# Performance work log

Hardware: AMD Instinct MI355X
Metric: run time of the kernel (lower is better)

Reference implementation:

```python
import jax, jax.numpy as jnp
import numpy as np

# Config values (from c.mean_shift / c.cuda in the original module)
EMBED_DIM = 32      # embedding_dim
BW = 2.0            # kernel_bandwidth
ETA = 0.5           # step_size
N_ITERS = 3         # nb_iterations
RES = 96            # pic_res (image is RES x RES, N = RES*RES pixels)


def setup_inputs() -> dict:
    key = jax.random.key(0)
    # Scale 0.1 keeps exp(BW * x^T x) well inside fp32 range, mimicking the
    # bounded embeddings produced by the upstream margin-loss-trained net.
    x_in = 0.1 * jax.random.normal(key, (1, EMBED_DIM, RES, RES), dtype=jnp.float32)
    return {"x_in": x_in}


def reference(x_in):
    # x_in: (1, D, RES, RES). One mean-shift step per iteration:
    #   K = exp(bw * X^T X)                      (N x N affinity)
    #   deg_j = sum_i K[i, j]                    (column degree; K is symmetric)
    #   X_new = eta * X @ (K / deg) + (1-eta) * X
    # (The original's torch.inverse(diag(deg)) is exactly 1/deg column scaling.)
    # All iterates are concatenated along dim 0, as in the torch code.
    res = x_in.shape[3]
    n = res * res
    xs = [x_in.reshape(EMBED_DIM, n)]
    for _ in range(N_ITERS):
        X = xs[-1]                                    # (D, N)
        K = jnp.exp(BW * jnp.einsum('di,dj->ij', X, X))  # (N, N)
        deg = K.sum(axis=0)                           # (N,) column sums
        xs.append(ETA * (X @ (K / deg)) + (1.0 - ETA) * X)
    # (N_ITERS+1, D, RES, RES)
    return jnp.stack(xs, axis=0).reshape(-1, EMBED_DIM, res, res)
```

## Files before the change

kernel.cpp:

```cpp
#include <hip/hip_runtime.h>
#include <hip/hip_bf16.h>


#define DIM 32
#define RESO 96
#define NPT (RESO * RESO)
#define NITER 3
#define ETA 0.5f
#define SCALE 2.88539008f

#define QB 144
#define NQB (NPT / QB)
#define NG 9
#define KSEG 4
#define CHUNK 256
#define NCHUNK (NPT / CHUNK)

typedef __bf16 bf16_t;
typedef __bf16 v8bf __attribute__((ext_vector_type(8)));
typedef float  v4f  __attribute__((ext_vector_type(4)));

__device__ __forceinline__ int keyinv(int m) {
    return ((m & 8) << 1) | ((m & 4) << 1) | ((m & 16) >> 2) | (m & 3);
}

__global__ __launch_bounds__(256, 4)
void pack_kernel(const float* __restrict__ X,
                 bf16_t* __restrict__ rows,
                 bf16_t* __restrict__ rows_s,
                 bf16_t* __restrict__ cols,
                 float* __restrict__ out_copy) {
    __shared__ float tt[32][33];
    const int tid = threadIdx.x;
    const int n0  = blockIdx.x * 32;
    const int inv = keyinv(tid & 31);

#pragma unroll
    for (int j = 0; j < 4; ++j) {
        int d = (tid >> 5) + j * 8;
        int n = tid & 31;
        float v = X[(size_t)d * NPT + n0 + n];
        tt[d][n] = v;
        cols[(size_t)d * NPT + n0 + inv] = (bf16_t)v;
        out_copy[(size_t)d * NPT + n0 + n] = v;
    }
    __syncthreads();

#pragma unroll
    for (int j = 0; j < 4; ++j) {
        int n = (tid >> 5) + j * 8;
        int d = tid & 31;
        float v = tt[d][n];
        rows[(size_t)(n0 + n) * DIM + d]   = (bf16_t)v;
        rows_s[(size_t)(n0 + n) * DIM + d] = (bf16_t)(v * SCALE);
    }
}

__global__ __launch_bounds__(512, 2)
void msattn_kernel(const bf16_t* __restrict__ rows,
                   const bf16_t* __restrict__ rows_s,
                   const bf16_t* __restrict__ cols,
                   float* __restrict__ part_num,
                   float* __restrict__ part_den) {
    __shared__ float osum[8][48][33];
    __shared__ float dsum[8][QB];

    const int tid  = threadIdx.x;
    const int w    = tid >> 6;
    const int lane = tid & 63;
    const int quad = lane >> 4;
    const int l16  = lane & 15;
    const int qb   = blockIdx.x;
    const int ks   = blockIdx.y;
    const int c0   = ks * (NCHUNK / KSEG);
    const int c1   = c0 + (NCHUNK / KSEG);
    const int q0   = qb * QB;

    v8bf qf[NG];
#pragma unroll
    for (int g = 0; g < NG; ++g)
        qf[g] = *(const v8bf*)&rows_s[(size_t)(q0 + g * 16 + l16) * DIM + quad * 8];

    v8bf ones;
#pragma unroll
    for (int j = 0; j < 8; ++j) ones[j] = (bf16_t)1.0f;

    const bf16_t* pA = rows + ((size_t)(c0 * CHUNK + w * 32 + l16)) * DIM + quad * 8;
    const bf16_t* pB = cols + (size_t)l16 * NPT + c0 * CHUNK + w * 32 + quad * 8;

    v4f acc[NG][2];
    v4f den[NG];
#pragma unroll
    for (int g = 0; g < NG; ++g) {
        acc[g][0] = (v4f){0.f, 0.f, 0.f, 0.f};
        acc[g][1] = (v4f){0.f, 0.f, 0.f, 0.f};
        den[g]    = (v4f){0.f, 0.f, 0.f, 0.f};
    }

    v8bf ka0 = *(const v8bf*)pA;
    v8bf ka1 = *(const v8bf*)(pA + 16 * DIM);
    v8bf bV0 = *(const v8bf*)pB;
    v8bf bV1 = *(const v8bf*)(pB + (size_t)16 * NPT);
    pA += CHUNK * DIM;
    pB += CHUNK;

    for (int c = c0; c < c1; ++c) {
        const bool more = (c + 1 < c1);
        v8bf nka0, nka1, nb0, nb1;
        if (more) {
            nka0 = *(const v8bf*)pA;
            nka1 = *(const v8bf*)(pA + 16 * DIM);
            nb0  = *(const v8bf*)pB;
            nb1  = *(const v8bf*)(pB + (size_t)16 * NPT);
            pA += CHUNK * DIM;
            pB += CHUNK;
        }

#pragma unroll
        for (int g = 0; g < NG; ++g) {
            v4f s0 = __builtin_amdgcn_mfma_f32_16x16x32_bf16(ka0, qf[g],
                         (v4f){0.f, 0.f, 0.f, 0.f}, 0, 0, 0);
            v4f s1 = __builtin_amdgcn_mfma_f32_16x16x32_bf16(ka1, qf[g],
                         (v4f){0.f, 0.f, 0.f, 0.f}, 0, 0, 0);
            v8bf pa;
#pragma unroll
            for (int r = 0; r < 4; ++r) {
                pa[r]     = (bf16_t)__builtin_amdgcn_exp2f(s0[r]);
                pa[4 + r] = (bf16_t)__builtin_amdgcn_exp2f(s1[r]);
            }
            acc[g][0] = __builtin_amdgcn_mfma_f32_16x16x32_bf16(pa, bV0, acc[g][0], 0, 0, 0);
            acc[g][1] = __builtin_amdgcn_mfma_f32_16x16x32_bf16(pa, bV1, acc[g][1], 0, 0, 0);
            den[g]    = __builtin_amdgcn_mfma_f32_16x16x32_bf16(pa, ones, den[g], 0, 0, 0);
        }

        if (more) { ka0 = nka0; ka1 = nka1; bV0 = nb0; bV1 = nb1; }
    }

    if (l16 == 0) {
#pragma unroll
        for (int g = 0; g < NG; ++g)
#pragma unroll
            for (int r = 0; r < 4; ++r)
                dsum[w][g * 16 + quad * 4 + r] = den[g][r];
    }

#pragma unroll
    for (int round = 0; round < 3; ++round) {
        if (round) __syncthreads();
#pragma unroll
        for (int gg = 0; gg < 3; ++gg) {
            int g = round * 3 + gg;
#pragma unroll
            for (int h = 0; h < 2; ++h)
#pragma unroll
                for (int r = 0; r < 4; ++r)
                    osum[w][gg * 16 + quad * 4 + r][h * 16 + l16] = acc[g][h][r];
        }
        __syncthreads();
#pragma unroll
        for (int e = 0; e < 3; ++e) {
            int idx = tid + e * 512;
            int qr = idx >> 5, d = idx & 31;
            float s = osum[0][qr][d] + osum[1][qr][d] + osum[2][qr][d]
                    + osum[3][qr][d] + osum[4][qr][d] + osum[5][qr][d]
                    + osum[6][qr][d] + osum[7][qr][d];
            part_num[((size_t)ks * NPT + q0 + round * 48 + qr) * DIM + d] = s;
        }
    }
    if (tid < QB) {
        float s = dsum[0][tid] + dsum[1][tid] + dsum[2][tid] + dsum[3][tid]
                + dsum[4][tid] + dsum[5][tid] + dsum[6][tid] + dsum[7][tid];
        part_den[ks * NPT + q0 + tid] = s;
    }
}

__global__ __launch_bounds__(512, 2)
void reduce_kernel(const float* __restrict__ part_num,
                   const float* __restrict__ part_den,
                   const float* __restrict__ Xcur,
                   float* __restrict__ Xnext,
                   bf16_t* __restrict__ rows_out,
                   bf16_t* __restrict__ rows_s_out,
                   bf16_t* __restrict__ cols_out) {
    __shared__ float tp[2][32][33];
    __shared__ float dpart[KSEG][32];
    __shared__ float txn[32][33];

    const int tid = threadIdx.x;
    const int q0  = blockIdx.x * 32;
    const int inv = keyinv(tid & 31);

    {
        int slot = tid & 255;
        int sh   = tid >> 8;
        int qq = slot >> 3, dq = slot & 7;
        const float* pb = &part_num[(size_t)(q0 + qq) * DIM + dq * 4];
        size_t seg = (size_t)NPT * DIM;
        v4f s = *(const v4f*)&pb[(2 * sh) * seg]
              + *(const v4f*)&pb[(2 * sh + 1) * seg];
#pragma unroll
        for (int k = 0; k < 4; ++k) tp[sh][qq][dq * 4 + k] = s[k];
    }
    if (tid < KSEG * 32) {
        int ss = tid >> 5, q = tid & 31;
        dpart[ss][q] = part_den[ss * NPT + q0 + q];
    }
    __syncthreads();

#pragma unroll
    for (int e = 0; e < 2; ++e) {
        int idx = tid + e * 512;
        int d = idx >> 5, qq = idx & 31;
        float num = tp[0][qq][d] + tp[1][qq][d];
        float dn = dpart[0][qq] + dpart[1][qq] + dpart[2][qq] + dpart[3][qq];
        float xo = Xcur[(size_t)d * NPT + q0 + qq];
        float xn = ETA * num / dn + (1.0f - ETA) * xo;
        Xnext[(size_t)d * NPT + q0 + qq] = xn;
        cols_out[(size_t)d * NPT + q0 + inv] = (bf16_t)xn;
        txn[qq][d] = xn;
    }
    __syncthreads();

#pragma unroll
    for (int e = 0; e < 2; ++e) {
        int idx = tid + e * 512;
        int qq = idx >> 5, d = idx & 31;
        float v = txn[qq][d];
        rows_out[(size_t)(q0 + qq) * DIM + d]   = (bf16_t)v;
        rows_s_out[(size_t)(q0 + qq) * DIM + d] = (bf16_t)(v * SCALE);
    }
}

extern "C" void kernel_launch(void* const* d_in, const int* in_sizes, int n_in,
                              void* d_out, int out_size, void* d_ws, size_t ws_size,
                              hipStream_t stream) {
    const float* x_in = (const float*)d_in[0];
    float* out = (float*)d_out;

    const size_t DN = (size_t)DIM * NPT;
    bf16_t* rows0  = (bf16_t*)d_ws;
    bf16_t* rowss0 = rows0 + DN;
    bf16_t* cols0  = rowss0 + DN;
    bf16_t* rows1  = cols0 + DN;
    bf16_t* rowss1 = rows1 + DN;
    bf16_t* cols1  = rowss1 + DN;
    float* part_num = (float*)(cols1 + DN);
    float* part_den = part_num + (size_t)KSEG * NPT * DIM;

    pack_kernel<<<NPT / 32, 256, 0, stream>>>(x_in, rows0, rowss0, cols0, out);

    for (int it = 0; it < NITER; ++it) {
        const float* Xcur = (it == 0) ? x_in : out + (size_t)it * DN;
        bf16_t* rin   = (it & 1) ? rows1 : rows0;
        bf16_t* rsin  = (it & 1) ? rowss1 : rowss0;
        bf16_t* cin   = (it & 1) ? cols1 : cols0;
        bf16_t* rout  = (it & 1) ? rows0 : rows1;
        bf16_t* rsout = (it & 1) ? rowss0 : rowss1;
        bf16_t* cout  = (it & 1) ? cols0 : cols1;
        msattn_kernel<<<dim3(NQB, KSEG), 512, 0, stream>>>(rin, rsin, cin,
                                                           part_num, part_den);
        reduce_kernel<<<NPT / 32, 512, 0, stream>>>(part_num, part_den, Xcur,
                                                    out + (size_t)(it + 1) * DN,
                                                    rout, rsout, cout);
    }
}
```

Baseline: 124.3 us.

## Fuse pack, attention and reduce launches into one cooperative persistent kernel

Replaces the seven separate launches (pack, then three attention/reduce pairs) with a single cooperative kernel of 256 blocks that separates phases with grid-wide syncs. This removes per-launch overhead and the gaps between kernels. On the last iteration it also skips writing the bf16 row and column copies, which nothing reads afterwards. In exchange the work per phase is tied to a fixed grid of 256 blocks, grid.sync costs are added, and shared memory per block grows because every phase's buffers are held at once, which may lower occupancy.

```diff
diff --git a/kernel.cpp b/kernel.cpp
--- a/kernel.cpp
+++ b/kernel.cpp
@@ -1,5 +1,8 @@
 #include <hip/hip_runtime.h>
 #include <hip/hip_bf16.h>
+#include <hip/hip_cooperative_groups.h>
+
+namespace cg = cooperative_groups;
 
 
 #define DIM 32
@@ -15,6 +18,8 @@
 #define KSEG 4
 #define CHUNK 256
 #define NCHUNK (NPT / CHUNK)
+#define NBLK 256
+#define NTILE (NPT / 32)
 
 typedef __bf16 bf16_t;
 typedef __bf16 v8bf __attribute__((ext_vector_type(8)));
@@ -24,210 +29,223 @@
     return ((m & 8) << 1) | ((m & 4) << 1) | ((m & 16) >> 2) | (m & 3);
 }
 
-__global__ __launch_bounds__(256, 4)
-void pack_kernel(const float* __restrict__ X,
-                 bf16_t* __restrict__ rows,
-                 bf16_t* __restrict__ rows_s,
-                 bf16_t* __restrict__ cols,
-                 float* __restrict__ out_copy) {
-    __shared__ float tt[32][33];
-    const int tid = threadIdx.x;
-    const int n0  = blockIdx.x * 32;
-    const int inv = keyinv(tid & 31);
-
-#pragma unroll
-    for (int j = 0; j < 4; ++j) {
-        int d = (tid >> 5) + j * 8;
-        int n = tid & 31;
-        float v = X[(size_t)d * NPT + n0 + n];
-        tt[d][n] = v;
-        cols[(size_t)d * NPT + n0 + inv] = (bf16_t)v;
-        out_copy[(size_t)d * NPT + n0 + n] = v;
-    }
-    __syncthreads();
-
-#pragma unroll
-    for (int j = 0; j < 4; ++j) {
-        int n = (tid >> 5) + j * 8;
-        int d = tid & 31;
-        float v = tt[d][n];
-        rows[(size_t)(n0 + n) * DIM + d]   = (bf16_t)v;
-        rows_s[(size_t)(n0 + n) * DIM + d] = (bf16_t)(v * SCALE);
-    }
-}
-
 __global__ __launch_bounds__(512, 2)
-void msattn_kernel(const bf16_t* __restrict__ rows,
-                   const bf16_t* __restrict__ rows_s,
-                   const bf16_t* __restrict__ cols,
-                   float* __restrict__ part_num,
-                   float* __restrict__ part_den) {
+void mega_kernel(const float* __restrict__ x_in,
+                 bf16_t* __restrict__ rows0, bf16_t* __restrict__ rowss0,
+                 bf16_t* __restrict__ cols0,
+                 bf16_t* __restrict__ rows1, bf16_t* __restrict__ rowss1,
+                 bf16_t* __restrict__ cols1,
+                 float* __restrict__ part_num,
+                 float* __restrict__ part_den,
+                 float* __restrict__ out) {
     __shared__ float osum[8][48][33];
     __shared__ float dsum[8][QB];
+    __shared__ float tt[32][33];
+    __shared__ float tp[2][32][33];
+    __shared__ float dpart[KSEG][32];
+    __shared__ float txn[32][33];
+
+    cg::grid_group grid = cg::this_grid();
 
     const int tid  = threadIdx.x;
+    const int bid  = blockIdx.x;
     const int w    = tid >> 6;
     const int lane = tid & 63;
     const int quad = lane >> 4;
     const int l16  = lane & 15;
-    const int qb   = blockIdx.x;
-    const int ks   = blockIdx.y;
-    const int c0   = ks * (NCHUNK / KSEG);
-    const int c1   = c0 + (NCHUNK / KSEG);
-    const int q0   = qb * QB;
-
-    v8bf qf[NG];
-#pragma unroll
-    for (int g = 0; g < NG; ++g)
-        qf[g] = *(const v8bf*)&rows_s[(size_t)(q0 + g * 16 + l16) * DIM + quad * 8];
-
-    v8bf ones;
-#pragma unroll
-    for (int j = 0; j < 8; ++j) ones[j] = (bf16_t)1.0f;
-
-    const bf16_t* pA = rows + ((size_t)(c0 * CHUNK + w * 32 + l16)) * DIM + quad * 8;
-    const bf16_t* pB = cols + (size_t)l16 * NPT + c0 * CHUNK + w * 32 + quad * 8;
-
-    v4f acc[NG][2];
-    v4f den[NG];
-#pragma unroll
-    for (int g = 0; g < NG; ++g) {
-        acc[g][0] = (v4f){0.f, 0.f, 0.f, 0.f};
-        acc[g][1] = (v4f){0.f, 0.f, 0.f, 0.f};
-        den[g]    = (v4f){0.f, 0.f, 0.f, 0.f};
+    const int inv  = keyinv(tid & 31);
+    const size_t DN = (size_t)DIM * NPT;
+
+    for (int tile = bid; tile < NTILE; tile += NBLK) {
+        const int n0 = tile * 32;
+#pragma unroll
+        for (int j = 0; j < 2; ++j) {
+            int d = (tid >> 5) + j * 16;
+            int n = tid & 31;
+            float v = x_in[(size_t)d * NPT + n0 + n];
+            tt[d][n] = v;
+            cols0[(size_t)d * NPT + n0 + inv] = (bf16_t)v;
+            out[(size_t)d * NPT + n0 + n] = v;
+        }
+        __syncthreads();
+#pragma unroll
+        for (int j = 0; j < 2; ++j) {
+            int n = (tid >> 5) + j * 16;
+            int d = tid & 31;
+            float v = tt[d][n];
+            rows0[(size_t)(n0 + n) * DIM + d]   = (bf16_t)v;
+            rowss0[(size_t)(n0 + n) * DIM + d] = (bf16_t)(v * SCALE);
+        }
+        __syncthreads();
     }
-
-    v8bf ka0 = *(const v8bf*)pA;
-    v8bf ka1 = *(const v8bf*)(pA + 16 * DIM);
-    v8bf bV0 = *(const v8bf*)pB;
-    v8bf bV1 = *(const v8bf*)(pB + (size_t)16 * NPT);
-    pA += CHUNK * DIM;
-    pB += CHUNK;
-
-    for (int c = c0; c < c1; ++c) {
-        const bool more = (c + 1 < c1);
-        v8bf nka0, nka1, nb0, nb1;
-        if (more) {
-            nka0 = *(const v8bf*)pA;
-            nka1 = *(const v8bf*)(pA + 16 * DIM);
-            nb0  = *(const v8bf*)pB;
-            nb1  = *(const v8bf*)(pB + (size_t)16 * NPT);
+    grid.sync();
+
+    for (int it = 0; it < NITER; ++it) {
+        const bf16_t* rin  = (it & 1) ? rows1 : rows0;
+        const bf16_t* rsin = (it & 1) ? rowss1 : rowss0;
+        const bf16_t* cin  = (it & 1) ? cols1 : cols0;
+        bf16_t* rout  = (it & 1) ? rows0 : rows1;
+        bf16_t* rsout = (it & 1) ? rowss0 : rowss1;
+        bf16_t* cout  = (it & 1) ? cols0 : cols1;
+        const float* Xcur = out + (size_t)it * DN;
+        float* Xnext      = out + (size_t)(it + 1) * DN;
+
+        {
+            const int qb = bid & 63;
+            const int ks = bid >> 6;
+            const int c0 = ks * (NCHUNK / KSEG);
+            const int c1 = c0 + (NCHUNK / KSEG);
+            const int q0 = qb * QB;
+
+            v8bf qf[NG];
+#pragma unroll
+            for (int g = 0; g < NG; ++g)
+                qf[g] = *(const v8bf*)&rsin[(size_t)(q0 + g * 16 + l16) * DIM + quad * 8];
+
+            v8bf ones;
+#pragma unroll
+            for (int j = 0; j < 8; ++j) ones[j] = (bf16_t)1.0f;
+
+            const bf16_t* pA = rin + ((size_t)(c0 * CHUNK + w * 32 + l16)) * DIM + quad * 8;
+            const bf16_t* pB = cin + (size_t)l16 * NPT + c0 * CHUNK + w * 32 + quad * 8;
+
+            v4f acc[NG][2];
+            v4f den[NG];
+#pragma unroll
+            for (int g = 0; g < NG; ++g) {
+                acc[g][0] = (v4f){0.f, 0.f, 0.f, 0.f};
+                acc[g][1] = (v4f){0.f, 0.f, 0.f, 0.f};
+                den[g]    = (v4f){0.f, 0.f, 0.f, 0.f};
+            }
+
+            v8bf ka0 = *(const v8bf*)pA;
+            v8bf ka1 = *(const v8bf*)(pA + 16 * DIM);
+            v8bf bV0 = *(const v8bf*)pB;
+            v8bf bV1 = *(const v8bf*)(pB + (size_t)16 * NPT);
             pA += CHUNK * DIM;
             pB += CHUNK;
-        }
-
-#pragma unroll
-        for (int g = 0; g < NG; ++g) {
-            v4f s0 = __builtin_amdgcn_mfma_f32_16x16x32_bf16(ka0, qf[g],
-                         (v4f){0.f, 0.f, 0.f, 0.f}, 0, 0, 0);
-            v4f s1 = __builtin_amdgcn_mfma_f32_16x16x32_bf16(ka1, qf[g],
-                         (v4f){0.f, 0.f, 0.f, 0.f}, 0, 0, 0);
-            v8bf pa;
-#pragma unroll
-            for (int r = 0; r < 4; ++r) {
-                pa[r]     = (bf16_t)__builtin_amdgcn_exp2f(s0[r]);
-                pa[4 + r] = (bf16_t)__builtin_amdgcn_exp2f(s1[r]);
-            }
-            acc[g][0] = __builtin_amdgcn_mfma_f32_16x16x32_bf16(pa, bV0, acc[g][0], 0, 0, 0);
-            acc[g][1] = __builtin_amdgcn_mfma_f32_16x16x32_bf16(pa, bV1, acc[g][1], 0, 0, 0);
-            den[g]    = __builtin_amdgcn_mfma_f32_16x16x32_bf16(pa, ones, den[g], 0, 0, 0);
-        }
-
-        if (more) { ka0 = nka0; ka1 = nka1; bV0 = nb0; bV1 = nb1; }
-    }
-
-    if (l16 == 0) {
-#pragma unroll
-        for (int g = 0; g < NG; ++g)
-#pragma unroll
-            for (int r = 0; r < 4; ++r)
-                dsum[w][g * 16 + quad * 4 + r] = den[g][r];
-    }
-
-#pragma unroll
-    for (int round = 0; round < 3; ++round) {
-        if (round) __syncthreads();
-#pragma unroll
-        for (int gg = 0; gg < 3; ++gg) {
-            int g = round * 3 + gg;
-#pragma unroll
-            for (int h = 0; h < 2; ++h)
-#pragma unroll
-                for (int r = 0; r < 4; ++r)
-                    osum[w][gg * 16 + quad * 4 + r][h * 16 + l16] = acc[g][h][r];
-        }
-        __syncthreads();
-#pragma unroll
-        for (int e = 0; e < 3; ++e) {
-            int idx = tid + e * 512;
-            int qr = idx >> 5, d = idx & 31;
-            float s = osum[0][qr][d] + osum[1][qr][d] + osum[2][qr][d]
-                    + osum[3][qr][d] + osum[4][qr][d] + osum[5][qr][d]
-                    + osum[6][qr][d] + osum[7][qr][d];
-            part_num[((size_t)ks * NPT + q0 + round * 48 + qr) * DIM + d] = s;
-        }
-    }
-    if (tid < QB) {
-        float s = dsum[0][tid] + dsum[1][tid] + dsum[2][tid] + dsum[3][tid]
-                + dsum[4][tid] + dsum[5][tid] + dsum[6][tid] + dsum[7][tid];
-        part_den[ks * NPT + q0 + tid] = s;
-    }
-}
-
-__global__ __launch_bounds__(512, 2)
-void reduce_kernel(const float* __restrict__ part_num,
-                   const float* __restrict__ part_den,
-                   const float* __restrict__ Xcur,
-                   float* __restrict__ Xnext,
-                   bf16_t* __restrict__ rows_out,
-                   bf16_t* __restrict__ rows_s_out,
-                   bf16_t* __restrict__ cols_out) {
-    __shared__ float tp[2][32][33];
-    __shared__ float dpart[KSEG][32];
-    __shared__ float txn[32][33];
-
-    const int tid = threadIdx.x;
-    const int q0  = blockIdx.x * 32;
-    const int inv = keyinv(tid & 31);
-
-    {
-        int slot = tid & 255;
-        int sh   = tid >> 8;
-        int qq = slot >> 3, dq = slot & 7;
-        const float* pb = &part_num[(size_t)(q0 + qq) * DIM + dq * 4];
-        size_t seg = (size_t)NPT * DIM;
-        v4f s = *(const v4f*)&pb[(2 * sh) * seg]
-              + *(const v4f*)&pb[(2 * sh + 1) * seg];
-#pragma unroll
-        for (int k = 0; k < 4; ++k) tp[sh][qq][dq * 4 + k] = s[k];
-    }
-    if (tid < KSEG * 32) {
-        int ss = tid >> 5, q = tid & 31;
-        dpart[ss][q] = part_den[ss * NPT + q0 + q];
-    }
-    __syncthreads();
-
-#pragma unroll
-    for (int e = 0; e < 2; ++e) {
-        int idx = tid + e * 512;
-        int d = idx >> 5, qq = idx & 31;
-        float num = tp[0][qq][d] + tp[1][qq][d];
-        float dn = dpart[0][qq] + dpart[1][qq] + dpart[2][qq] + dpart[3][qq];
-        float xo = Xcur[(size_t)d * NPT + q0 + qq];
-        float xn = ETA * num / dn + (1.0f - ETA) * xo;
-        Xnext[(size_t)d * NPT + q0 + qq] = xn;
-        cols_out[(size_t)d * NPT + q0 + inv] = (bf16_t)xn;
-        txn[qq][d] = xn;
-    }
-    __syncthreads();
-
-#pragma unroll
-    for (int e = 0; e < 2; ++e) {
-        int idx = tid + e * 512;
-        int qq = idx >> 5, d = idx & 31;
-        float v = txn[qq][d];
-        rows_out[(size_t)(q0 + qq) * DIM + d]   = (bf16_t)v;
-        rows_s_out[(size_t)(q0 + qq) * DIM + d] = (bf16_t)(v * SCALE);
+
+            for (int c = c0; c < c1; ++c) {
+                const bool more = (c + 1 < c1);
+                v8bf nka0, nka1, nb0, nb1;
+                if (more) {
+                    nka0 = *(const v8bf*)pA;
+                    nka1 = *(const v8bf*)(pA + 16 * DIM);
+                    nb0  = *(const v8bf*)pB;
+                    nb1  = *(const v8bf*)(pB + (size_t)16 * NPT);
+                    pA += CHUNK * DIM;
+                    pB += CHUNK;
+                }
+
+#pragma unroll
+                for (int g = 0; g < NG; ++g) {
+                    v4f s0 = __builtin_amdgcn_mfma_f32_16x16x32_bf16(ka0, qf[g],
+                                 (v4f){0.f, 0.f, 0.f, 0.f}, 0, 0, 0);
+                    v4f s1 = __builtin_amdgcn_mfma_f32_16x16x32_bf16(ka1, qf[g],
+                                 (v4f){0.f, 0.f, 0.f, 0.f}, 0, 0, 0);
+                    v8bf pa;
+#pragma unroll
+                    for (int r = 0; r < 4; ++r) {
+                        pa[r]     = (bf16_t)__builtin_amdgcn_exp2f(s0[r]);
+                        pa[4 + r] = (bf16_t)__builtin_amdgcn_exp2f(s1[r]);
+                    }
+                    acc[g][0] = __builtin_amdgcn_mfma_f32_16x16x32_bf16(pa, bV0, acc[g][0], 0, 0, 0);
+                    acc[g][1] = __builtin_amdgcn_mfma_f32_16x16x32_bf16(pa, bV1, acc[g][1], 0, 0, 0);
+                    den[g]    = __builtin_amdgcn_mfma_f32_16x16x32_bf16(pa, ones, den[g], 0, 0, 0);
+                }
+
+                if (more) { ka0 = nka0; ka1 = nka1; bV0 = nb0; bV1 = nb1; }
+            }
+
+            if (l16 == 0) {
+#pragma unroll
+                for (int g = 0; g < NG; ++g)
+#pragma unroll
+                    for (int r = 0; r < 4; ++r)
+                        dsum[w][g * 16 + quad * 4 + r] = den[g][r];
+            }
+
+#pragma unroll
+            for (int round = 0; round < 3; ++round) {
+                if (round) __syncthreads();
+#pragma unroll
+                for (int gg = 0; gg < 3; ++gg) {
+                    int g = round * 3 + gg;
+#pragma unroll
+                    for (int h = 0; h < 2; ++h)
+#pragma unroll
+                        for (int r = 0; r < 4; ++r)
+                            osum[w][gg * 16 + quad * 4 + r][h * 16 + l16] = acc[g][h][r];
+                }
+                __syncthreads();
+#pragma unroll
+                for (int e = 0; e < 3; ++e) {
+                    int idx = tid + e * 512;
+                    int qr = idx >> 5, d = idx & 31;
+                    float s = osum[0][qr][d] + osum[1][qr][d] + osum[2][qr][d]
+                            + osum[3][qr][d] + osum[4][qr][d] + osum[5][qr][d]
+                            + osum[6][qr][d] + osum[7][qr][d];
+                    part_num[((size_t)ks * NPT + q0 + round * 48 + qr) * DIM + d] = s;
+                }
+            }
+            if (tid < QB) {
+                float s = dsum[0][tid] + dsum[1][tid] + dsum[2][tid] + dsum[3][tid]
+                        + dsum[4][tid] + dsum[5][tid] + dsum[6][tid] + dsum[7][tid];
+                part_den[ks * NPT + q0 + tid] = s;
+            }
+            __syncthreads();
+        }
+        grid.sync();
+
+        const bool last = (it == NITER - 1);
+        for (int tile = bid; tile < NTILE; tile += NBLK) {
+            const int q0 = tile * 32;
+
+            {
+                int slot = tid & 255;
+                int sh   = tid >> 8;
+                int qq = slot >> 3, dq = slot & 7;
+                const float* pb = &part_num[(size_t)(q0 + qq) * DIM + dq * 4];
+                size_t seg = (size_t)NPT * DIM;
+                v4f s = *(const v4f*)&pb[(2 * sh) * seg]
+                      + *(const v4f*)&pb[(2 * sh + 1) * seg];
+#pragma unroll
+                for (int k = 0; k < 4; ++k) tp[sh][qq][dq * 4 + k] = s[k];
+            }
+            if (tid < KSEG * 32) {
+                int ss = tid >> 5, q = tid & 31;
+                dpart[ss][q] = part_den[ss * NPT + q0 + q];
+            }
+            __syncthreads();
+
+#pragma unroll
+            for (int e = 0; e < 2; ++e) {
+                int idx = tid + e * 512;
+                int d = idx >> 5, qq = idx & 31;
+                float num = tp[0][qq][d] + tp[1][qq][d];
+                float dn = dpart[0][qq] + dpart[1][qq] + dpart[2][qq] + dpart[3][qq];
+                float xo = Xcur[(size_t)d * NPT + q0 + qq];
+                float xn = ETA * num / dn + (1.0f - ETA) * xo;
+                Xnext[(size_t)d * NPT + q0 + qq] = xn;
+                if (!last) cols_store: ;
+                if (!last) cout[(size_t)d * NPT + q0 + inv] = (bf16_t)xn;
+                txn[qq][d] = xn;
+            }
+            __syncthreads();
+
+            if (!last) {
+#pragma unroll
+                for (int e = 0; e < 2; ++e) {
+                    int idx = tid + e * 512;
+                    int qq = idx >> 5, d = idx & 31;
+                    float v = txn[qq][d];
+                    rout[(size_t)(q0 + qq) * DIM + d]  = (bf16_t)v;
+                    rsout[(size_t)(q0 + qq) * DIM + d] = (bf16_t)(v * SCALE);
+                }
+            }
+            __syncthreads();
+        }
+        if (!last) grid.sync();
     }
 }
 
@@ -247,20 +265,13 @@
     float* part_num = (float*)(cols1 + DN);
     float* part_den = part_num + (size_t)KSEG * NPT * DIM;
 
-    pack_kernel<<<NPT / 32, 256, 0, stream>>>(x_in, rows0, rowss0, cols0, out);
-
-    for (int it = 0; it < NITER; ++it) {
-        const float* Xcur = (it == 0) ? x_in : out + (size_t)it * DN;
-        bf16_t* rin   = (it & 1) ? rows1 : rows0;
-        bf16_t* rsin  = (it & 1) ? rowss1 : rowss0;
-        bf16_t* cin   = (it & 1) ? cols1 : cols0;
-        bf16_t* rout  = (it & 1) ? rows0 : rows1;
-        bf16_t* rsout = (it & 1) ? rowss0 : rowss1;
-        bf16_t* cout  = (it & 1) ? cols0 : cols1;
-        msattn_kernel<<<dim3(NQB, KSEG), 512, 0, stream>>>(rin, rsin, cin,
-                                                           part_num, part_den);
-        reduce_kernel<<<NPT / 32, 512, 0, stream>>>(part_num, part_den, Xcur,
-                                                    out + (size_t)(it + 1) * DN,
-                                                    rout, rsout, cout);
-    }
+    void* args[] = {
+        (void*)&x_in,
+        (void*)&rows0, (void*)&rowss0, (void*)&cols0,
+        (void*)&rows1, (void*)&rowss1, (void*)&cols1,
+        (void*)&part_num, (void*)&part_den,
+        (void*)&out
+    };
+    hipLaunchCooperativeKernel((const void*)mega_kernel, dim3(NBLK), dim3(512),
+                               args, 0, stream);
 }
```

New measurement: 303.4 us. +144.0%, slower.
